# Optimization experiments

Hardware: AMD Instinct MI355X
Metric: run time of the kernel (lower is better)

The kernel has to match this reference:

```python
import jax, jax.numpy as jnp
import numpy as np

B, T, F, H, FW = 4096, 200, 32, 8, 5  # batch, seq, features, hidden, forward_size


def setup_inputs() -> dict:
    key = jax.random.key(0)
    ks = jax.random.split(key, 12)
    s_ih = 1.0 / np.sqrt(F + 1)
    s_hh = 1.0 / np.sqrt(H)
    inp = {
        "x": jax.random.normal(ks[0], (B, T, F), dtype=jnp.float32),
        "z0": jax.random.uniform(ks[1], (1, B, 1), dtype=jnp.float32),
        # LSTM cell over concat([x_t, z_{t-1}]) -> hidden 8, torch gate order i,f,g,o
        "W_ih": jax.random.uniform(ks[2], (4 * H, F + 1), minval=-s_ih, maxval=s_ih),
        "W_hh": jax.random.uniform(ks[3], (4 * H, H), minval=-s_hh, maxval=s_hh),
        "b_ih": jax.random.uniform(ks[4], (4 * H,), minval=-s_hh, maxval=s_hh),
        "b_hh": jax.random.uniform(ks[5], (4 * H,), minval=-s_hh, maxval=s_hh),
        # forward head: 8 -> 5 (relu, dropout inert at inference) -> 1 (relu, monotone increment)
        "W1": jax.random.uniform(ks[6], (FW, H), minval=-s_hh, maxval=s_hh),
        "b1": jax.random.uniform(ks[7], (FW,), minval=-s_hh, maxval=s_hh),
        "W2": jax.random.uniform(ks[8], (1, FW), minval=-1 / np.sqrt(FW), maxval=1 / np.sqrt(FW)),
        "b2": jax.random.uniform(ks[9], (1,), minval=-1 / np.sqrt(FW), maxval=1 / np.sqrt(FW)),
    }
    return inp


def _monotonic_lstm(x, z0, W_ih, W_hh, b_ih, b_hh, W1, b1, W2, b2):
    Bloc = x.shape[0]
    h0 = jnp.zeros((Bloc, H), x.dtype)
    c0 = jnp.zeros((Bloc, H), x.dtype)
    z = z0[0]  # (B, 1) : drop num_layers dim
    bias = b_ih + b_hh

    def step(carry, xt):
        h, c, z = carry
        inp = jnp.concatenate([xt, z], axis=-1)  # (B, F+1)
        gates = inp @ W_ih.T + h @ W_hh.T + bias  # (B, 4H)
        i, f, g, o = jnp.split(gates, 4, axis=-1)
        c = jax.nn.sigmoid(f) * c + jax.nn.sigmoid(i) * jnp.tanh(g)
        h = jax.nn.sigmoid(o) * jnp.tanh(c)
        d = jax.nn.relu(h @ W1.T + b1)            # dropout is identity at inference
        delta = jax.nn.relu(d @ W2.T + b2)        # nonnegative increment -> monotone z
        z = z + delta
        return (h, c, z), z

    _, zs = jax.lax.scan(step, (h0, c0, z), jnp.swapaxes(x, 0, 1))  # zs: (T, B, 1)
    return jnp.swapaxes(zs, 0, 1)  # (B, T, 1)


def reference(x, z0, W_ih, W_hh, b_ih, b_hh, W1, b1, W2, b2):
    return _monotonic_lstm(x, z0, W_ih, W_hh, b_ih, b_hh, W1, b1, W2, b2)
```

## Files before the change

kernel.cpp:

```cpp
#include <hip/hip_runtime.h>

#define T_LEN 200
#define F_IN  32
#define TC    8
#define NCH   (T_LEN / TC)
#define NB    8
#define PSTR  264
#define ZSTR  204

#define QP(a,b,c,d) ((a)|((b)<<2)|((c)<<4)|((d)<<6))
#define DPP_HM 0x141

typedef short  bf16x8  __attribute__((ext_vector_type(8)));
typedef float  floatx4 __attribute__((ext_vector_type(4)));

template <int CTRL>
__device__ __forceinline__ float dppf(float v) {
    return __int_as_float(__builtin_amdgcn_update_dpp(
        0, __float_as_int(v), CTRL, 0xF, 0xF, true));
}
__device__ __forceinline__ void bfsplit(float x, short& hi, short& lo) {
    unsigned u = __float_as_uint(x);
    unsigned short h = (unsigned short)(u >> 16);
    float fh = __uint_as_float(((unsigned)h) << 16);
    float r  = x - fh;
    hi = (short)h;
    lo = (short)(__float_as_uint(r) >> 16);
}

__launch_bounds__(128, 1)
__global__ void mono_lstm_kernel(const float* __restrict__ x,
                                 const float* __restrict__ z0,
                                 const float* __restrict__ W_ih,
                                 const float* __restrict__ W_hh,
                                 const float* __restrict__ b_ih,
                                 const float* __restrict__ b_hh,
                                 const float* __restrict__ W1,
                                 const float* __restrict__ b1,
                                 const float* __restrict__ W2,
                                 const float* __restrict__ b2,
                                 float* __restrict__ out) {
    __shared__ float pls[2 * NB * PSTR];
    __shared__ float zls[NB * ZSTR];

    const int tid  = threadIdx.x;
    const int lane = tid & 63;
    const int wv   = tid >> 6;
    const int bl   = lane >> 3;
    const int j    = lane & 7;
    const int bg   = blockIdx.x * NB;

    const float L2E = 1.4426950408889634f;
    const float NSC = -L2E;
    const float NSG = -2.0f * L2E;

    const int n  = lane & 15;
    const int kq = lane >> 4;
    bf16x8 Bh0, Bl0, Bh1, Bl1;
    float bias0 = 0.f, bias1 = 0.f;

    const int   am  = lane & 15;
    const float* xa = x + ((size_t)(bg + (am >> 1)) * T_LEN + (am & 1)) * F_IN + kq * 8;

    float4 rgv[8];
    auto load_x = [&](int ch) {
#pragma unroll
        for (int s = 0; s < 4; ++s) {
            const float* p = xa + (size_t)(ch * TC + 2 * s) * F_IN;
            rgv[2 * s]     = *(const float4*)p;
            rgv[2 * s + 1] = *(const float4*)(p + 4);
        }
    };
    auto mfma_phase = [&](int buf) {
#pragma unroll
        for (int s = 0; s < 4; ++s) {
            const float xv[8] = {rgv[2*s].x, rgv[2*s].y, rgv[2*s].z, rgv[2*s].w,
                                 rgv[2*s+1].x, rgv[2*s+1].y, rgv[2*s+1].z, rgv[2*s+1].w};
            bf16x8 Ah, Al;
#pragma unroll
            for (int i = 0; i < 8; ++i) {
                short h, l;
                bfsplit(xv[i], h, l);
                Ah[i] = h; Al[i] = l;
            }
            floatx4 a0 = {bias0, bias0, bias0, bias0};
            floatx4 a1 = {bias1, bias1, bias1, bias1};
            a0 = __builtin_amdgcn_mfma_f32_16x16x32_bf16(Ah, Bh0, a0, 0, 0, 0);
            a0 = __builtin_amdgcn_mfma_f32_16x16x32_bf16(Al, Bh0, a0, 0, 0, 0);
            a0 = __builtin_amdgcn_mfma_f32_16x16x32_bf16(Ah, Bl0, a0, 0, 0, 0);
            a1 = __builtin_amdgcn_mfma_f32_16x16x32_bf16(Ah, Bh1, a1, 0, 0, 0);
            a1 = __builtin_amdgcn_mfma_f32_16x16x32_bf16(Al, Bh1, a1, 0, 0, 0);
            a1 = __builtin_amdgcn_mfma_f32_16x16x32_bf16(Ah, Bl1, a1, 0, 0, 0);
#pragma unroll
            for (int reg = 0; reg < 4; ++reg) {
                const int mr = (lane >> 4) * 4 + reg;
                const int bb = mr >> 1, tt = 2 * s + (mr & 1);
                pls[buf * NB * PSTR + bb * PSTR + tt * 32 + n]      = a0[reg];
                pls[buf * NB * PSTR + bb * PSTR + tt * 32 + 16 + n] = a1[reg];
            }
        }
    };

    float whi[8], whf[8], whg[8], who[8];
    float wzi = 0.f, wzf = 0.f, wzg = 0.f, wzo = 0.f;
    float w1own[8];
    float b1own = 0.f, w2own = 0.f, b2v = 0.f;
    float ha0 = 0.f, ha1 = 0.f, ha2 = 0.f, ha3 = 0.f,
          ha4 = 0.f, ha5 = 0.f, ha6 = 0.f, ha7 = 0.f;
    float c = 0.0f;
    float z = 0.f;
    float zk = 0.f;
#pragma unroll
    for (int k = 0; k < 8; ++k) w1own[k] = 0.f;

    if (wv == 1) {
        const int row0 = n, row1 = 16 + n;
        const float sc0 = NSC;
        const float sc1 = (n < 8) ? NSG : NSC;
#pragma unroll
        for (int i = 0; i < 8; ++i) {
            const int k = kq * 8 + i;
            short h, l;
            bfsplit(W_ih[row0 * 33 + k] * sc0, h, l); Bh0[i] = h; Bl0[i] = l;
            bfsplit(W_ih[row1 * 33 + k] * sc1, h, l); Bh1[i] = h; Bl1[i] = l;
        }
        bias0 = (b_ih[row0] + b_hh[row0]) * sc0;
        bias1 = (b_ih[row1] + b_hh[row1]) * sc1;

        load_x(0);
        mfma_phase(0);
        load_x(1);
    } else {
        const int ri = j, rf = 8 + j, rg_ = 16 + j, ro = 24 + j;
#pragma unroll
        for (int k = 0; k < 8; ++k) {
            whi[k] = W_hh[ri * 8 + (j ^ k)] * NSC;
            whf[k] = W_hh[rf * 8 + (j ^ k)] * NSC;
            whg[k] = W_hh[rg_ * 8 + (j ^ k)] * NSG;
            who[k] = W_hh[ro * 8 + (j ^ k)] * NSC;
        }
        wzi = W_ih[ri * 33 + 32] * NSC;
        wzf = W_ih[rf * 33 + 32] * NSC;
        wzg = W_ih[rg_ * 33 + 32] * NSG;
        wzo = W_ih[ro * 33 + 32] * NSC;

        if (j < 5) {
#pragma unroll
            for (int k = 0; k < 8; ++k) w1own[k] = W1[j * 8 + (j ^ k)];
            b1own = b1[j];
            w2own = W2[j];
        }
        b2v = b2[0];
        z = z0[bg + bl];
    }

    __syncthreads();

    for (int ch = 0; ch < NCH; ++ch) {
        if (wv == 1) {
            if (ch + 1 < NCH) {
                mfma_phase((ch + 1) & 1);
                if (ch + 2 < NCH) load_x(ch + 2);
            }
        } else {
            const int base = (ch & 1) * NB * PSTR + bl * PSTR;
            float pvi[TC], pvf[TC], pvg[TC], pvo[TC];
#pragma unroll
            for (int t = 0; t < TC; ++t) {
                pvi[t] = pls[base + t * 32 + j];
                pvf[t] = pls[base + t * 32 + 8 + j];
                pvg[t] = pls[base + t * 32 + 16 + j];
                pvo[t] = pls[base + t * 32 + 24 + j];
            }

#pragma unroll
            for (int t = 0; t < TC; ++t) {
                float mi = fmaf(whi[0], ha0, fmaf(whi[1], ha1,
                           fmaf(whi[2], ha2, fmaf(whi[3], ha3, pvi[t]))));
                float ni = fmaf(whi[4], ha4, fmaf(whi[5], ha5,
                           fmaf(whi[6], ha6, whi[7] * ha7)));
                float mf = fmaf(whf[0], ha0, fmaf(whf[1], ha1,
                           fmaf(whf[2], ha2, fmaf(whf[3], ha3, pvf[t]))));
                float nf = fmaf(whf[4], ha4, fmaf(whf[5], ha5,
                           fmaf(whf[6], ha6, whf[7] * ha7)));
                float mg = fmaf(whg[0], ha0, fmaf(whg[1], ha1,
                           fmaf(whg[2], ha2, fmaf(whg[3], ha3, pvg[t]))));
                float ng = fmaf(whg[4], ha4, fmaf(whg[5], ha5,
                           fmaf(whg[6], ha6, whg[7] * ha7)));
                float mo = fmaf(who[0], ha0, fmaf(who[1], ha1,
                           fmaf(who[2], ha2, fmaf(who[3], ha3, pvo[t]))));
                float no = fmaf(who[4], ha4, fmaf(who[5], ha5,
                           fmaf(who[6], ha6, who[7] * ha7)));

                const float ai = fmaf(wzi, z, mi + ni);
                const float af = fmaf(wzf, z, mf + nf);
                const float ag = fmaf(wzg, z, mg + ng);
                const float ao = fmaf(wzo, z, mo + no);

                const float si = __builtin_amdgcn_rcpf(1.0f + __builtin_amdgcn_exp2f(ai));
                const float sf = __builtin_amdgcn_rcpf(1.0f + __builtin_amdgcn_exp2f(af));
                const float sg = __builtin_amdgcn_rcpf(1.0f + __builtin_amdgcn_exp2f(ag));
                const float so = __builtin_amdgcn_rcpf(1.0f + __builtin_amdgcn_exp2f(ao));
                const float tg = fmaf(2.0f, sg, -1.0f);

                c = fmaf(sf, c, si * tg);
                const float ec = __builtin_amdgcn_exp2f(c * (-2.0f * L2E));
                const float tc = fmaf(2.0f, __builtin_amdgcn_rcpf(1.0f + ec), -1.0f);
                const float hn = so * tc;

                ha0 = hn;
                ha1 = dppf<QP(1, 0, 3, 2)>(hn);
                ha2 = dppf<QP(2, 3, 0, 1)>(hn);
                ha3 = dppf<QP(3, 2, 1, 0)>(hn);
                const float t7 = dppf<DPP_HM>(hn);
                ha7 = t7;
                ha4 = dppf<QP(3, 2, 1, 0)>(t7);
                ha5 = dppf<QP(2, 3, 0, 1)>(t7);
                ha6 = dppf<QP(1, 0, 3, 2)>(t7);

                float da = fmaf(w1own[2], ha2, fmaf(w1own[1], ha1,
                           fmaf(w1own[0], ha0, b1own)));
                float db = fmaf(w1own[5], ha5, fmaf(w1own[4], ha4, w1own[3] * ha3));
                float dc = fmaf(w1own[7], ha7, w1own[6] * ha6);
                const float d = fmaxf((da + db) + dc, 0.0f);
                const float e = w2own * d;

                float q = e;
                q += dppf<QP(1, 0, 3, 2)>(q);
                q += dppf<QP(2, 3, 0, 1)>(q);
                q += dppf<DPP_HM>(q);

                z += fmaxf(q + b2v, 0.0f);
                zk = (j == t) ? z : zk;
            }
            zls[bl * ZSTR + ch * TC + j] = zk;
        }
        __syncthreads();
    }

#pragma unroll
    for (int it = 0; it < 4; ++it) {
        const int idx = tid + it * 128;
        if (idx < NB * (T_LEN / 4)) {
            const int bb = idx / 50, rem = idx - bb * 50;
            *(float4*)&out[(size_t)(bg + bb) * T_LEN + rem * 4] =
                *(const float4*)&zls[bb * ZSTR + rem * 4];
        }
    }
}

extern "C" void kernel_launch(void* const* d_in, const int* in_sizes, int n_in,
                              void* d_out, int out_size, void* d_ws, size_t ws_size,
                              hipStream_t stream) {
    const float* x    = (const float*)d_in[0];
    const float* z0   = (const float*)d_in[1];
    const float* W_ih = (const float*)d_in[2];
    const float* W_hh = (const float*)d_in[3];
    const float* b_ih = (const float*)d_in[4];
    const float* b_hh = (const float*)d_in[5];
    const float* W1   = (const float*)d_in[6];
    const float* b1   = (const float*)d_in[7];
    const float* W2   = (const float*)d_in[8];
    const float* b2   = (const float*)d_in[9];
    float* out = (float*)d_out;

    const int B = in_sizes[1];
    dim3 grid(B / NB), block(128);
    hipLaunchKernelGGL(mono_lstm_kernel, grid, block, 0, stream,
                       x, z0, W_ih, W_hh, b_ih, b_hh, W1, b1, W2, b2, out);
}
```

Before: 177.2 us.

## Pack gate math into float2 ops, vectorize LDS gate loads, fuse sigmoid-tanh reciprocals

Reorders the LDS layout of precomputed input projections so each lane reads its four gates as one float4 instead of four scalar loads. The recurrent matvec is expressed with two-wide float vectors so the compiler can emit packed FMA instructions. The product sigmoid(i)*tanh(g) is rewritten to use a single reciprocal of (1+eI)(1+eG), and the cell state is kept pre-scaled by -2*log2(e) so tanh(c) needs no extra multiply. These changes target the serial per-timestep dependency chain, at the cost of slightly different rounding and possible overflow when the product of the two denominators grows large.

```diff
diff --git a/kernel.cpp b/kernel.cpp
--- a/kernel.cpp
+++ b/kernel.cpp
@@ -10,9 +10,12 @@
 
 #define QP(a,b,c,d) ((a)|((b)<<2)|((c)<<4)|((d)<<6))
 #define DPP_HM 0x141
+#define EX2(v) __builtin_amdgcn_exp2f(v)
+#define RCP(v) __builtin_amdgcn_rcpf(v)
 
 typedef short  bf16x8  __attribute__((ext_vector_type(8)));
 typedef float  floatx4 __attribute__((ext_vector_type(4)));
+typedef float  floatx2 __attribute__((ext_vector_type(2)));
 
 template <int CTRL>
 __device__ __forceinline__ float dppf(float v) {
@@ -53,6 +56,7 @@
     const float L2E = 1.4426950408889634f;
     const float NSC = -L2E;
     const float NSG = -2.0f * L2E;
+    const float CPK =  2.0f * L2E;
 
     const int n  = lane & 15;
     const int kq = lane >> 4;
@@ -61,6 +65,9 @@
 
     const int   am  = lane & 15;
     const float* xa = x + ((size_t)(bg + (am >> 1)) * T_LEN + (am & 1)) * F_IN + kq * 8;
+
+    const int p0 = (n < 8) ? 4 * n : 4 * (n - 8) + 1;
+    const int p1 = (n < 8) ? 4 * n + 2 : 4 * (n - 8) + 3;
 
     float4 rgv[8];
     auto load_x = [&](int ch) {
@@ -95,23 +102,23 @@
             for (int reg = 0; reg < 4; ++reg) {
                 const int mr = (lane >> 4) * 4 + reg;
                 const int bb = mr >> 1, tt = 2 * s + (mr & 1);
-                pls[buf * NB * PSTR + bb * PSTR + tt * 32 + n]      = a0[reg];
-                pls[buf * NB * PSTR + bb * PSTR + tt * 32 + 16 + n] = a1[reg];
+                pls[buf * NB * PSTR + bb * PSTR + tt * 32 + p0] = a0[reg];
+                pls[buf * NB * PSTR + bb * PSTR + tt * 32 + p1] = a1[reg];
             }
         }
     };
 
-    float whi[8], whf[8], whg[8], who[8];
-    float wzi = 0.f, wzf = 0.f, wzg = 0.f, wzo = 0.f;
+    floatx2 wif[8], wgo[8];
+    floatx2 wzif = {0.f, 0.f}, wzgo = {0.f, 0.f};
     float w1own[8];
     float b1own = 0.f, w2own = 0.f, b2v = 0.f;
     float ha0 = 0.f, ha1 = 0.f, ha2 = 0.f, ha3 = 0.f,
           ha4 = 0.f, ha5 = 0.f, ha6 = 0.f, ha7 = 0.f;
-    float c = 0.0f;
+    float ck = 0.0f;
     float z = 0.f;
     float zk = 0.f;
 #pragma unroll
-    for (int k = 0; k < 8; ++k) w1own[k] = 0.f;
+    for (int k = 0; k < 8; ++k) { w1own[k] = 0.f; wif[k] = (floatx2){0.f, 0.f}; wgo[k] = (floatx2){0.f, 0.f}; }
 
     if (wv == 1) {
         const int row0 = n, row1 = 16 + n;
@@ -134,15 +141,13 @@
         const int ri = j, rf = 8 + j, rg_ = 16 + j, ro = 24 + j;
 #pragma unroll
         for (int k = 0; k < 8; ++k) {
-            whi[k] = W_hh[ri * 8 + (j ^ k)] * NSC;
-            whf[k] = W_hh[rf * 8 + (j ^ k)] * NSC;
-            whg[k] = W_hh[rg_ * 8 + (j ^ k)] * NSG;
-            who[k] = W_hh[ro * 8 + (j ^ k)] * NSC;
-        }
-        wzi = W_ih[ri * 33 + 32] * NSC;
-        wzf = W_ih[rf * 33 + 32] * NSC;
-        wzg = W_ih[rg_ * 33 + 32] * NSG;
-        wzo = W_ih[ro * 33 + 32] * NSC;
+            wif[k] = (floatx2){W_hh[ri * 8 + (j ^ k)] * NSC,
+                               W_hh[rf * 8 + (j ^ k)] * NSC};
+            wgo[k] = (floatx2){W_hh[rg_ * 8 + (j ^ k)] * NSG,
+                               W_hh[ro * 8 + (j ^ k)] * NSC};
+        }
+        wzif = (floatx2){W_ih[ri * 33 + 32] * NSC, W_ih[rf * 33 + 32] * NSC};
+        wzgo = (floatx2){W_ih[rg_ * 33 + 32] * NSG, W_ih[ro * 33 + 32] * NSC};
 
         if (j < 5) {
 #pragma unroll
@@ -164,49 +169,42 @@
             }
         } else {
             const int base = (ch & 1) * NB * PSTR + bl * PSTR;
-            float pvi[TC], pvf[TC], pvg[TC], pvo[TC];
+            float4 pq[TC];
+#pragma unroll
+            for (int t = 0; t < TC; ++t)
+                pq[t] = *(const float4*)&pls[base + t * 32 + 4 * j];
+
 #pragma unroll
             for (int t = 0; t < TC; ++t) {
-                pvi[t] = pls[base + t * 32 + j];
-                pvf[t] = pls[base + t * 32 + 8 + j];
-                pvg[t] = pls[base + t * 32 + 16 + j];
-                pvo[t] = pls[base + t * 32 + 24 + j];
-            }
-
-#pragma unroll
-            for (int t = 0; t < TC; ++t) {
-                float mi = fmaf(whi[0], ha0, fmaf(whi[1], ha1,
-                           fmaf(whi[2], ha2, fmaf(whi[3], ha3, pvi[t]))));
-                float ni = fmaf(whi[4], ha4, fmaf(whi[5], ha5,
-                           fmaf(whi[6], ha6, whi[7] * ha7)));
-                float mf = fmaf(whf[0], ha0, fmaf(whf[1], ha1,
-                           fmaf(whf[2], ha2, fmaf(whf[3], ha3, pvf[t]))));
-                float nf = fmaf(whf[4], ha4, fmaf(whf[5], ha5,
-                           fmaf(whf[6], ha6, whf[7] * ha7)));
-                float mg = fmaf(whg[0], ha0, fmaf(whg[1], ha1,
-                           fmaf(whg[2], ha2, fmaf(whg[3], ha3, pvg[t]))));
-                float ng = fmaf(whg[4], ha4, fmaf(whg[5], ha5,
-                           fmaf(whg[6], ha6, whg[7] * ha7)));
-                float mo = fmaf(who[0], ha0, fmaf(who[1], ha1,
-                           fmaf(who[2], ha2, fmaf(who[3], ha3, pvo[t]))));
-                float no = fmaf(who[4], ha4, fmaf(who[5], ha5,
-                           fmaf(who[6], ha6, who[7] * ha7)));
-
-                const float ai = fmaf(wzi, z, mi + ni);
-                const float af = fmaf(wzf, z, mf + nf);
-                const float ag = fmaf(wzg, z, mg + ng);
-                const float ao = fmaf(wzo, z, mo + no);
-
-                const float si = __builtin_amdgcn_rcpf(1.0f + __builtin_amdgcn_exp2f(ai));
-                const float sf = __builtin_amdgcn_rcpf(1.0f + __builtin_amdgcn_exp2f(af));
-                const float sg = __builtin_amdgcn_rcpf(1.0f + __builtin_amdgcn_exp2f(ag));
-                const float so = __builtin_amdgcn_rcpf(1.0f + __builtin_amdgcn_exp2f(ao));
-                const float tg = fmaf(2.0f, sg, -1.0f);
-
-                c = fmaf(sf, c, si * tg);
-                const float ec = __builtin_amdgcn_exp2f(c * (-2.0f * L2E));
-                const float tc = fmaf(2.0f, __builtin_amdgcn_rcpf(1.0f + ec), -1.0f);
-                const float hn = so * tc;
+                const floatx2 z2  = {z, z};
+                const floatx2 hb0 = {ha0, ha0}, hb1 = {ha1, ha1},
+                              hb2 = {ha2, ha2}, hb3 = {ha3, ha3},
+                              hb4 = {ha4, ha4}, hb5 = {ha5, ha5},
+                              hb6 = {ha6, ha6}, hb7 = {ha7, ha7};
+                const floatx2 pIF = {pq[t].x, pq[t].y};
+                const floatx2 pGO = {pq[t].z, pq[t].w};
+
+                floatx2 mIF = wif[0]*hb0 + (wif[1]*hb1 + (wif[2]*hb2 + (wif[3]*hb3 + pIF)));
+                floatx2 nIF = wif[4]*hb4 + (wif[5]*hb5 + (wif[6]*hb6 + wif[7]*hb7));
+                floatx2 aIF = wzif*z2 + (mIF + nIF);
+                floatx2 mGO = wgo[0]*hb0 + (wgo[1]*hb1 + (wgo[2]*hb2 + (wgo[3]*hb3 + pGO)));
+                floatx2 nGO = wgo[4]*hb4 + (wgo[5]*hb5 + (wgo[6]*hb6 + wgo[7]*hb7));
+                floatx2 aGO = wzgo*z2 + (mGO + nGO);
+
+                const float eI = EX2(aIF.x), eF = EX2(aIF.y);
+                const float eG = EX2(aGO.x), eO = EX2(aGO.y);
+
+                const float sf  = RCP(1.0f + eF);
+                const float so  = RCP(1.0f + eO);
+                const float den = (1.0f + eI) * (1.0f + eG);
+                const float r   = RCP(den);
+                const float numK = fmaf(CPK, eG, NSG);
+                const float sitgK = r * numK;
+                ck = fmaf(sf, ck, sitgK);
+                const float ec  = EX2(ck);
+                const float rc  = RCP(1.0f + ec);
+                const float so2 = so + so;
+                const float hn  = fmaf(so2, rc, -so);
 
                 ha0 = hn;
                 ha1 = dppf<QP(1, 0, 3, 2)>(hn);
```

After: 174.4 us. About the same (-1.6%).
